# Kernel optimization log

Hardware: AMD Instinct MI355X
Metric: run time of the kernel (lower is better)

The kernel has to match this reference:

```python
import jax, jax.numpy as jnp
import numpy as np

B, IN, OUT, HS, NBDA = 128, 256, 256, 512, 1

def setup_inputs() -> dict:
    key = jax.random.key(0)
    ks = jax.random.split(key, 16)
    d = {}
    d["inputs"] = jax.random.normal(ks[0], (B, IN), dtype=jnp.float32)
    d["hidden"] = jax.random.normal(ks[1], (B, HS), dtype=jnp.float32)
    d["hebb"] = jax.random.normal(ks[2], (B, HS, HS), dtype=jnp.float32) * 0.1
    # learned params (torch.nn.Linear: y = x @ W.T + b)
    d["i2h_w"] = jax.random.normal(ks[3], (HS, IN), dtype=jnp.float32) * (1.0 / np.sqrt(IN))
    d["i2h_b"] = jnp.zeros((HS,), dtype=jnp.float32)
    d["w"] = 0.01 * jax.random.uniform(ks[4], (HS, HS), dtype=jnp.float32)
    d["alpha"] = 0.01 * jax.random.uniform(ks[5], (HS, HS), dtype=jnp.float32)
    d["h2o_w"] = jax.random.normal(ks[6], (OUT, HS), dtype=jnp.float32) * (1.0 / np.sqrt(HS))
    d["h2o_b"] = jnp.zeros((OUT,), dtype=jnp.float32)
    d["h2v_w"] = jax.random.normal(ks[7], (1, HS), dtype=jnp.float32) * (1.0 / np.sqrt(HS))
    d["h2v_b"] = jnp.zeros((1,), dtype=jnp.float32)
    d["h2da_w"] = jax.random.normal(ks[8], (NBDA, HS), dtype=jnp.float32) * (1.0 / np.sqrt(HS))
    d["h2da_b"] = jnp.zeros((NBDA,), dtype=jnp.float32)
    return d

def reference(inputs, hidden, hebb, i2h_w, i2h_b, w, alpha, h2o_w, h2o_b,
              h2v_w, h2v_b, h2da_w, h2da_b):
    # hactiv = tanh(i2h(x) + (w + alpha*hebb) @ hidden), per-sample weight matrix
    pre = inputs @ i2h_w.T + i2h_b                              # [B, HS]
    w_eff = w + alpha * hebb                                    # [B, HS, HS]
    rec = jnp.einsum('bij,bj->bi', w_eff, hidden)               # [B, HS]
    hactiv = jnp.tanh(pre + rec)                                # [B, HS]
    activout = hactiv @ h2o_w.T + h2o_b                         # [B, OUT]
    valueout = hactiv @ h2v_w.T + h2v_b                         # [B, 1]
    da = jnp.tanh(hactiv @ h2da_w.T + h2da_b)                   # [B, NBDA]
    # outer-product Hebbian update, DA-modulated, clamped to [-1, 1]
    deltahebb = hactiv[:, :, None] * hidden[:, None, :]         # [B, HS, HS]
    hebb_new = jnp.clip(hebb + da[:, :1, None] * deltahebb, -1.0, 1.0)
    return activout, valueout, hactiv, hebb_new
```

## Files before the change

### kernel.cpp

```cpp
#include <hip/hip_runtime.h>
#include <cstddef>
#include <cstdint>

#define B_    128
#define IN_   256
#define OUT_  256
#define HS_   512

#define NTHR_  512
#define NBLK_  1024

__device__ __forceinline__ float clip1(float x) {
    return fminf(fmaxf(x, -1.f), 1.f);
}

typedef float f32x4 __attribute__((ext_vector_type(4)));
__device__ __forceinline__ void nt_store4(float4* p, float4 v) {
    __builtin_nontemporal_store(*(f32x4*)&v, (f32x4*)p);
}

__global__ __launch_bounds__(NTHR_, 4) void k_pass1(
    const float* __restrict__ inputs,
    const float* __restrict__ hidden,
    const float* __restrict__ hebb,
    const float* __restrict__ i2h_w,
    const float* __restrict__ i2h_b,
    const float* __restrict__ w,
    const float* __restrict__ alpha,
    const float* __restrict__ h2v_w,
    const float* __restrict__ h2da_w,
    float* __restrict__ hactiv,
    float* __restrict__ ws_pd,
    float* __restrict__ ws_pv)
{
    const int blk  = blockIdx.x;
    const int b    = blk >> 3;
    const int s    = blk & 7;
    const int tid  = threadIdx.x;
    const int wave = tid >> 6;
    const int lane = tid & 63;
    const int r0   = s * 64 + wave * 8;

    __shared__ float s_pd[8], s_pv[8];

    const float4* hid4 = (const float4*)(hidden + (size_t)b * HS_);
    const float4 h0  = hid4[lane];
    const float4 h1  = hid4[lane + 64];
    const float4 in4 = ((const float4*)(inputs + (size_t)b * IN_))[lane];

    const float4* hb4 = (const float4*)hebb + ((size_t)b * HS_) * (HS_ / 4);
    const float4* w4  = (const float4*)w;
    const float4* a4  = (const float4*)alpha;
    const float4* iw4 = (const float4*)i2h_w;

    float pd = 0.f, pv = 0.f;
    for (int t = 0; t < 8; t += 2) {
        const int i = r0 + t;
        const float4* hpA = hb4 + (size_t)i * (HS_ / 4);
        const float4* hpB = hpA + (HS_ / 4);
        const float4* wpA = w4  + (size_t)i * (HS_ / 4);
        const float4* apA = a4  + (size_t)i * (HS_ / 4);
        const float4* ipA = iw4 + (size_t)i * (IN_ / 4);

        const float4 xA0 = hpA[lane],            xA1 = hpA[lane + 64];
        const float4 xB0 = hpB[lane],            xB1 = hpB[lane + 64];
        const float4 wA0 = wpA[lane],            wA1 = wpA[lane + 64];
        const float4 wB0 = wpA[128 + lane],      wB1 = wpA[128 + lane + 64];
        const float4 aA0 = apA[lane],            aA1 = apA[lane + 64];
        const float4 aB0 = apA[128 + lane],      aB1 = apA[128 + lane + 64];
        const float4 iA  = ipA[lane];
        const float4 iB  = ipA[64 + lane];

        float a, c;
        a  = (wA0.x + aA0.x * xA0.x) * h0.x;
        a += (wA0.y + aA0.y * xA0.y) * h0.y;
        a += (wA0.z + aA0.z * xA0.z) * h0.z;
        a += (wA0.w + aA0.w * xA0.w) * h0.w;
        a += (wA1.x + aA1.x * xA1.x) * h1.x;
        a += (wA1.y + aA1.y * xA1.y) * h1.y;
        a += (wA1.z + aA1.z * xA1.z) * h1.z;
        a += (wA1.w + aA1.w * xA1.w) * h1.w;
        a += iA.x * in4.x + iA.y * in4.y + iA.z * in4.z + iA.w * in4.w;

        c  = (wB0.x + aB0.x * xB0.x) * h0.x;
        c += (wB0.y + aB0.y * xB0.y) * h0.y;
        c += (wB0.z + aB0.z * xB0.z) * h0.z;
        c += (wB0.w + aB0.w * xB0.w) * h0.w;
        c += (wB1.x + aB1.x * xB1.x) * h1.x;
        c += (wB1.y + aB1.y * xB1.y) * h1.y;
        c += (wB1.z + aB1.z * xB1.z) * h1.z;
        c += (wB1.w + aB1.w * xB1.w) * h1.w;
        c += iB.x * in4.x + iB.y * in4.y + iB.z * in4.z + iB.w * in4.w;

        #pragma unroll
        for (int off = 1; off < 64; off <<= 1) {
            a += __shfl_xor(a, off, 64);
            c += __shfl_xor(c, off, 64);
        }

        const float hA = tanhf(a + i2h_b[i]);
        const float hB = tanhf(c + i2h_b[i + 1]);
        if (lane == 0) {
            float2* hp = (float2*)(hactiv + (size_t)b * HS_ + i);
            *hp = make_float2(hA, hB);
            pd += hA * h2da_w[i] + hB * h2da_w[i + 1];
            pv += hA * h2v_w[i]  + hB * h2v_w[i + 1];
        }
    }

    if (lane == 0) { s_pd[wave] = pd; s_pv[wave] = pv; }
    __syncthreads();
    if (tid == 0) {
        float sd = 0.f, sv = 0.f;
        #pragma unroll
        for (int k = 0; k < 8; ++k) { sd += s_pd[k]; sv += s_pv[k]; }
        ws_pd[b * 8 + s] = sd;
        ws_pv[b * 8 + s] = sv;
    }
}

__global__ __launch_bounds__(NTHR_, 4) void k_pass2(
    const float* __restrict__ hidden,
    const float* __restrict__ hebb,
    const float* __restrict__ h2o_w,
    const float* __restrict__ h2o_b,
    const float* __restrict__ h2v_b,
    const float* __restrict__ h2da_b,
    const float* __restrict__ hactiv,
    float* __restrict__ activout,
    float* __restrict__ valueout,
    float* __restrict__ hebb_new,
    const float* __restrict__ ws_pd,
    const float* __restrict__ ws_pv)
{
    const int blk  = blockIdx.x;
    const int b    = blk >> 3;
    const int s    = blk & 7;
    const int tid  = threadIdx.x;
    const int wave = tid >> 6;
    const int lane = tid & 63;
    const int r0   = s * 64 + wave * 8;

    __shared__ float s_h[HS_];
    __shared__ float s_part[512];
    __shared__ float s_bc[1];

    if (tid < 128)
        ((float4*)s_h)[tid] = ((const float4*)(hactiv + (size_t)b * HS_))[tid];
    if (tid == 0) {
        float sd = 0.f, sv = 0.f;
        #pragma unroll
        for (int k = 0; k < 8; ++k) {
            sd += ws_pd[b * 8 + k];
            sv += ws_pv[b * 8 + k];
        }
        s_bc[0] = tanhf(sd + h2da_b[0]);
        if (s == 0)
            valueout[b] = sv + h2v_b[0];
    }
    __syncthreads();
    const float da_b = s_bc[0];

    const float4* hid4 = (const float4*)(hidden + (size_t)b * HS_);
    const float4 h0 = hid4[lane];
    const float4 h1 = hid4[lane + 64];

    const float4* hb4 = (const float4*)hebb + ((size_t)b * HS_) * (HS_ / 4);

    for (int t = 0; t < 8; t += 2) {
        const int i = r0 + t;
        const float4* xp = hb4 + (size_t)i * (HS_ / 4);
        const float4 x0 = xp[lane],       x1 = xp[lane + 64];
        const float4 y0 = xp[128 + lane], y1 = xp[128 + lane + 64];
        const float scA = da_b * s_h[i];
        const float scB = da_b * s_h[i + 1];

        float4 o0, o1, p0, p1;
        o0.x = clip1(fmaf(scA, h0.x, x0.x));
        o0.y = clip1(fmaf(scA, h0.y, x0.y));
        o0.z = clip1(fmaf(scA, h0.z, x0.z));
        o0.w = clip1(fmaf(scA, h0.w, x0.w));
        o1.x = clip1(fmaf(scA, h1.x, x1.x));
        o1.y = clip1(fmaf(scA, h1.y, x1.y));
        o1.z = clip1(fmaf(scA, h1.z, x1.z));
        o1.w = clip1(fmaf(scA, h1.w, x1.w));
        p0.x = clip1(fmaf(scB, h0.x, y0.x));
        p0.y = clip1(fmaf(scB, h0.y, y0.y));
        p0.z = clip1(fmaf(scB, h0.z, y0.z));
        p0.w = clip1(fmaf(scB, h0.w, y0.w));
        p1.x = clip1(fmaf(scB, h1.x, y1.x));
        p1.y = clip1(fmaf(scB, h1.y, y1.y));
        p1.z = clip1(fmaf(scB, h1.z, y1.z));
        p1.w = clip1(fmaf(scB, h1.w, y1.w));

        float4* dp = (float4*)hebb_new + ((size_t)b * HS_ + i) * (HS_ / 4);
        nt_store4(dp + lane,            o0);
        nt_store4(dp + lane + 64,       o1);
        nt_store4(dp + 128 + lane,      p0);
        nt_store4(dp + 128 + lane + 64, p1);
    }

    {
        const int ol = tid & 31;
        const int sg = tid >> 5;
        const int o  = s * 32 + ol;
        const float4* wp  = (const float4*)(h2o_w + (size_t)o * HS_);
        const float4* hp4 = (const float4*)s_h;
        float acc = 0.f;
        #pragma unroll
        for (int c2 = 0; c2 < 8; ++c2) {
            const float4 wv = wp[sg * 8 + c2];
            const float4 hv = hp4[sg * 8 + c2];
            acc += wv.x * hv.x + wv.y * hv.y + wv.z * hv.z + wv.w * hv.w;
        }
        s_part[sg * 32 + ol] = acc;
    }
    __syncthreads();
    if (tid < 32) {
        const int o = s * 32 + tid;
        float acc = h2o_b[o];
        #pragma unroll
        for (int k = 0; k < 16; ++k)
            acc += s_part[k * 32 + tid];
        activout[(size_t)b * OUT_ + o] = acc;
    }
}

__global__ __launch_bounds__(256) void k1_hactiv(
    const float* __restrict__ inputs, const float* __restrict__ hidden,
    const float* __restrict__ hebb, const float* __restrict__ i2h_w,
    const float* __restrict__ i2h_b, const float* __restrict__ w,
    const float* __restrict__ alpha, float* __restrict__ hactiv)
{
    const int b     = blockIdx.x & (B_ - 1);
    const int chunk = blockIdx.x >> 7;
    const int tid   = threadIdx.x;
    const int wave  = tid >> 6;
    const int lane  = tid & 63;

    const float4* hid4 = (const float4*)(hidden + (size_t)b * HS_);
    const float4  h0   = hid4[lane];
    const float4  h1   = hid4[lane + 64];
    const float4  in4  = ((const float4*)(inputs + (size_t)b * IN_))[lane];

    const int i0 = chunk * 64 + wave * 16;

    for (int r = 0; r < 16; ++r) {
        const int i = i0 + r;
        const float4* hb = (const float4*)(hebb + ((size_t)b * HS_ + i) * HS_);
        const float4* wr = (const float4*)(w     + (size_t)i * HS_);
        const float4* ar = (const float4*)(alpha + (size_t)i * HS_);

        const float4 hb0 = hb[lane];
        const float4 hb1 = hb[lane + 64];
        const float4 wv0 = wr[lane];
        const float4 wv1 = wr[lane + 64];
        const float4 av0 = ar[lane];
        const float4 av1 = ar[lane + 64];
        const float4 iw  = ((const float4*)(i2h_w + (size_t)i * IN_))[lane];

        float acc;
        acc  = (wv0.x + av0.x * hb0.x) * h0.x;
        acc += (wv0.y + av0.y * hb0.y) * h0.y;
        acc += (wv0.z + av0.z * hb0.z) * h0.z;
        acc += (wv0.w + av0.w * hb0.w) * h0.w;
        acc += (wv1.x + av1.x * hb1.x) * h1.x;
        acc += (wv1.y + av1.y * hb1.y) * h1.y;
        acc += (wv1.z + av1.z * hb1.z) * h1.z;
        acc += (wv1.w + av1.w * hb1.w) * h1.w;
        acc += iw.x * in4.x + iw.y * in4.y + iw.z * in4.z + iw.w * in4.w;

        #pragma unroll
        for (int off = 32; off > 0; off >>= 1)
            acc += __shfl_down(acc, off, 64);

        if (lane == 0)
            hactiv[(size_t)b * HS_ + i] = tanhf(acc + i2h_b[i]);
    }
}

__global__ __launch_bounds__(256) void k2_heads(
    const float* __restrict__ hactiv, const float* __restrict__ h2o_w,
    const float* __restrict__ h2o_b, const float* __restrict__ h2v_w,
    const float* __restrict__ h2v_b, const float* __restrict__ h2da_w,
    const float* __restrict__ h2da_b, float* __restrict__ activout,
    float* __restrict__ valueout, float* __restrict__ da)
{
    const int b   = blockIdx.x;
    const int tid = threadIdx.x;

    __shared__ float s_h[HS_];
    __shared__ float red_v[256];
    __shared__ float red_d[256];

    for (int t = tid; t < HS_; t += 256)
        s_h[t] = hactiv[(size_t)b * HS_ + t];
    __syncthreads();

    const float4* wr  = (const float4*)(h2o_w + (size_t)tid * HS_);
    const float4* sh4 = (const float4*)s_h;
    float acc = 0.f;
    #pragma unroll 4
    for (int q = 0; q < HS_ / 4; ++q) {
        const float4 wv = wr[q];
        const float4 hv = sh4[q];
        acc += wv.x * hv.x + wv.y * hv.y + wv.z * hv.z + wv.w * hv.w;
    }
    activout[(size_t)b * OUT_ + tid] = acc + h2o_b[tid];

    float pv = 0.f, pd = 0.f;
    for (int t = tid; t < HS_; t += 256) {
        const float hv = s_h[t];
        pv += hv * h2v_w[t];
        pd += hv * h2da_w[t];
    }
    red_v[tid] = pv;
    red_d[tid] = pd;
    __syncthreads();
    for (int s2 = 128; s2 > 0; s2 >>= 1) {
        if (tid < s2) {
            red_v[tid] += red_v[tid + s2];
            red_d[tid] += red_d[tid + s2];
        }
        __syncthreads();
    }
    if (tid == 0) {
        valueout[b] = red_v[0] + h2v_b[0];
        da[b]       = tanhf(red_d[0] + h2da_b[0]);
    }
}

__global__ __launch_bounds__(256) void k3_hebb(
    const float* __restrict__ hebb, const float* __restrict__ hidden,
    const float* __restrict__ hactiv, const float* __restrict__ da,
    float* __restrict__ hebb_new)
{
    const int tid = threadIdx.x;
    const size_t base = (size_t)blockIdx.x * 1024;

    #pragma unroll
    for (int k = 0; k < 4; ++k) {
        const size_t idx = base + (size_t)k * 256 + tid;
        const int j4  = (int)(idx & 127);
        const int row = (int)(idx >> 7);
        const int i   = row & (HS_ - 1);
        const int b   = row >> 9;

        const float scale = da[b] * hactiv[(size_t)b * HS_ + i];
        const float4 hv = ((const float4*)hebb)[idx];
        const float4 hd = ((const float4*)hidden)[(size_t)b * (HS_ / 4) + j4];

        float4 r;
        r.x = fminf(fmaxf(fmaf(scale, hd.x, hv.x), -1.f), 1.f);
        r.y = fminf(fmaxf(fmaf(scale, hd.y, hv.y), -1.f), 1.f);
        r.z = fminf(fmaxf(fmaf(scale, hd.z, hv.z), -1.f), 1.f);
        r.w = fminf(fmaxf(fmaf(scale, hd.w, hv.w), -1.f), 1.f);
        ((float4*)hebb_new)[idx] = r;
    }
}

extern "C" void kernel_launch(void* const* d_in, const int* in_sizes, int n_in,
                              void* d_out, int out_size, void* d_ws, size_t ws_size,
                              hipStream_t stream)
{
    const float* inputs = (const float*)d_in[0];
    const float* hidden = (const float*)d_in[1];
    const float* hebb   = (const float*)d_in[2];
    const float* i2h_w  = (const float*)d_in[3];
    const float* i2h_b  = (const float*)d_in[4];
    const float* w      = (const float*)d_in[5];
    const float* alpha  = (const float*)d_in[6];
    const float* h2o_w  = (const float*)d_in[7];
    const float* h2o_b  = (const float*)d_in[8];
    const float* h2v_w  = (const float*)d_in[9];
    const float* h2v_b  = (const float*)d_in[10];
    const float* h2da_w = (const float*)d_in[11];
    const float* h2da_b = (const float*)d_in[12];

    float* out = (float*)d_out;
    float* activout = out;
    float* valueout = out + 32768;
    float* hactiv   = out + 32768 + 128;
    float* hebb_new = out + 32768 + 128 + 65536;

    const size_t part_bytes = (size_t)(2 * B_ * 8) * sizeof(float);

    if (ws_size >= part_bytes) {
        float* ws_pd = (float*)d_ws;
        float* ws_pv = ws_pd + B_ * 8;

        k_pass1<<<dim3(NBLK_), dim3(NTHR_), 0, stream>>>(
            inputs, hidden, hebb, i2h_w, i2h_b, w, alpha,
            h2v_w, h2da_w, hactiv, ws_pd, ws_pv);

        k_pass2<<<dim3(NBLK_), dim3(NTHR_), 0, stream>>>(
            hidden, hebb, h2o_w, h2o_b, h2v_b, h2da_b,
            hactiv, activout, valueout, hebb_new, ws_pd, ws_pv);
    } else {
        float* da = (float*)d_ws;
        k1_hactiv<<<dim3(1024), dim3(256), 0, stream>>>(
            inputs, hidden, hebb, i2h_w, i2h_b, w, alpha, hactiv);
        k2_heads<<<dim3(B_), dim3(256), 0, stream>>>(
            hactiv, h2o_w, h2o_b, h2v_w, h2v_b, h2da_w, h2da_b,
            activout, valueout, da);
        k3_hebb<<<dim3(8192), dim3(256), 0, stream>>>(
            hebb, hidden, hactiv, da, hebb_new);
    }
}
```

Measured before the change: 285.5 us.

## Hoist batch-shared W@h and i2h GEMM into tiled pre-kernel

Adds a small tiled GEMM kernel that computes i2h(x) + w@hidden once for the whole batch into a workspace buffer. The per-sample pass then only streams alpha and hebb, no longer rereading w and i2h_w in every block. This cuts redundant per-block loads of shared weights, at the cost of an extra launch and a low-occupancy 64-block GEMM. Pass2 also reads hactiv scalars from registers before the hebb loop and delays the shared-memory fill and barrier until after it. The new path only runs when the workspace is large enough; otherwise it falls back to the old fused pass1.

```diff
diff --git a/kernel.cpp b/kernel.cpp
--- a/kernel.cpp
+++ b/kernel.cpp
@@ -19,19 +19,154 @@
     __builtin_nontemporal_store(*(f32x4*)&v, (f32x4*)p);
 }
 
-__global__ __launch_bounds__(NTHR_, 4) void k_pass1(
+__global__ __launch_bounds__(256) void k0_pre(
     const float* __restrict__ inputs,
     const float* __restrict__ hidden,
-    const float* __restrict__ hebb,
     const float* __restrict__ i2h_w,
     const float* __restrict__ i2h_b,
     const float* __restrict__ w,
+    float* __restrict__ pre)
+{
+    const int it  = blockIdx.x & 15;
+    const int bt  = blockIdx.x >> 4;
+    const int tid = threadIdx.x;
+    const int il  = tid & 31;
+    const int bg  = tid >> 5;
+
+    __shared__ float Xl[32][68];
+    __shared__ float Wl[32][68];
+
+    float acc0 = 0.f, acc1 = 0.f, acc2 = 0.f, acc3 = 0.f;
+
+    for (int ck = 0; ck < 12; ++ck) {
+        __syncthreads();
+        #pragma unroll
+        for (int r = 0; r < 2; ++r) {
+            const int f   = tid + 256 * r;
+            const int row = f >> 4;
+            const int kf  = f & 15;
+            float4 xv, wv;
+            if (ck < 8) {
+                xv = *(const float4*)(hidden + (size_t)(bt*32 + row)*HS_ + ck*64 + kf*4);
+                wv = *(const float4*)(w      + (size_t)(it*32 + row)*HS_ + ck*64 + kf*4);
+            } else {
+                xv = *(const float4*)(inputs + (size_t)(bt*32 + row)*IN_ + (ck-8)*64 + kf*4);
+                wv = *(const float4*)(i2h_w  + (size_t)(it*32 + row)*IN_ + (ck-8)*64 + kf*4);
+            }
+            *(float4*)&Xl[row][kf*4] = xv;
+            *(float4*)&Wl[row][kf*4] = wv;
+        }
+        __syncthreads();
+        #pragma unroll
+        for (int kk = 0; kk < 64; ++kk) {
+            const float wv = Wl[il][kk];
+            acc0 = fmaf(wv, Xl[bg     ][kk], acc0);
+            acc1 = fmaf(wv, Xl[bg +  8][kk], acc1);
+            acc2 = fmaf(wv, Xl[bg + 16][kk], acc2);
+            acc3 = fmaf(wv, Xl[bg + 24][kk], acc3);
+        }
+    }
+
+    const int i = it * 32 + il;
+    const float bias = i2h_b[i];
+    pre[(size_t)(bt*32 + bg     ) * HS_ + i] = acc0 + bias;
+    pre[(size_t)(bt*32 + bg +  8) * HS_ + i] = acc1 + bias;
+    pre[(size_t)(bt*32 + bg + 16) * HS_ + i] = acc2 + bias;
+    pre[(size_t)(bt*32 + bg + 24) * HS_ + i] = acc3 + bias;
+}
+
+__global__ __launch_bounds__(NTHR_, 4) void k_pass1_slim(
+    const float* __restrict__ hidden,
+    const float* __restrict__ hebb,
     const float* __restrict__ alpha,
+    const float* __restrict__ pre,
     const float* __restrict__ h2v_w,
     const float* __restrict__ h2da_w,
     float* __restrict__ hactiv,
     float* __restrict__ ws_pd,
     float* __restrict__ ws_pv)
+{
+    const int blk  = blockIdx.x;
+    const int b    = blk >> 3;
+    const int s    = blk & 7;
+    const int tid  = threadIdx.x;
+    const int wave = tid >> 6;
+    const int lane = tid & 63;
+    const int r0   = s * 64 + wave * 8;
+
+    __shared__ float s_pd[8], s_pv[8];
+
+    const float4* hid4 = (const float4*)(hidden + (size_t)b * HS_);
+    const float4 h0 = hid4[lane];
+    const float4 h1 = hid4[lane + 64];
+
+    const float4* hb4 = (const float4*)hebb + ((size_t)b * HS_) * (HS_ / 4);
+    const float4* a4  = (const float4*)alpha;
+
+    float pd = 0.f, pv = 0.f;
+    for (int t = 0; t < 8; t += 2) {
+        const int i = r0 + t;
+        const float4* hpA = hb4 + (size_t)i * (HS_ / 4);
+        const float4* apA = a4  + (size_t)i * (HS_ / 4);
+
+        const float4 xA0 = hpA[lane],        xA1 = hpA[lane + 64];
+        const float4 xB0 = hpA[128 + lane],  xB1 = hpA[128 + lane + 64];
+        const float4 aA0 = apA[lane],        aA1 = apA[lane + 64];
+        const float4 aB0 = apA[128 + lane],  aB1 = apA[128 + lane + 64];
+
+        float a, c;
+        a  = (aA0.x * xA0.x) * h0.x;
+        a += (aA0.y * xA0.y) * h0.y;
+        a += (aA0.z * xA0.z) * h0.z;
+        a += (aA0.w * xA0.w) * h0.w;
+        a += (aA1.x * xA1.x) * h1.x;
+        a += (aA1.y * xA1.y) * h1.y;
+        a += (aA1.z * xA1.z) * h1.z;
+        a += (aA1.w * xA1.w) * h1.w;
+
+        c  = (aB0.x * xB0.x) * h0.x;
+        c += (aB0.y * xB0.y) * h0.y;
+        c += (aB0.z * xB0.z) * h0.z;
+        c += (aB0.w * xB0.w) * h0.w;
+        c += (aB1.x * xB1.x) * h1.x;
+        c += (aB1.y * xB1.y) * h1.y;
+        c += (aB1.z * xB1.z) * h1.z;
+        c += (aB1.w * xB1.w) * h1.w;
+
+        #pragma unroll
+        for (int off = 1; off < 64; off <<= 1) {
+            a += __shfl_xor(a, off, 64);
+            c += __shfl_xor(c, off, 64);
+        }
+
+        const float hA = tanhf(a + pre[(size_t)b * HS_ + i]);
+        const float hB = tanhf(c + pre[(size_t)b * HS_ + i + 1]);
+        if (lane == 0) {
+            float2* hp = (float2*)(hactiv + (size_t)b * HS_ + i);
+            *hp = make_float2(hA, hB);
+            pd += hA * h2da_w[i] + hB * h2da_w[i + 1];
+            pv += hA * h2v_w[i]  + hB * h2v_w[i + 1];
+        }
+    }
+
+    if (lane == 0) { s_pd[wave] = pd; s_pv[wave] = pv; }
+    __syncthreads();
+    if (tid == 0) {
+        float sd = 0.f, sv = 0.f;
+        #pragma unroll
+        for (int k = 0; k < 8; ++k) { sd += s_pd[k]; sv += s_pv[k]; }
+        ws_pd[b * 8 + s] = sd;
+        ws_pv[b * 8 + s] = sv;
+    }
+}
+
+__global__ __launch_bounds__(NTHR_, 4) void k_pass1_full(
+    const float* __restrict__ inputs, const float* __restrict__ hidden,
+    const float* __restrict__ hebb, const float* __restrict__ i2h_w,
+    const float* __restrict__ i2h_b, const float* __restrict__ w,
+    const float* __restrict__ alpha, const float* __restrict__ h2v_w,
+    const float* __restrict__ h2da_w, float* __restrict__ hactiv,
+    float* __restrict__ ws_pd, float* __restrict__ ws_pv)
 {
     const int blk  = blockIdx.x;
     const int b    = blk >> 3;
@@ -137,29 +272,27 @@
     const int b    = blk >> 3;
     const int s    = blk & 7;
     const int tid  = threadIdx.x;
+    const int lane = tid & 63;
     const int wave = tid >> 6;
-    const int lane = tid & 63;
     const int r0   = s * 64 + wave * 8;
 
     __shared__ float s_h[HS_];
     __shared__ float s_part[512];
-    __shared__ float s_bc[1];
-
-    if (tid < 128)
-        ((float4*)s_h)[tid] = ((const float4*)(hactiv + (size_t)b * HS_))[tid];
-    if (tid == 0) {
-        float sd = 0.f, sv = 0.f;
-        #pragma unroll
-        for (int k = 0; k < 8; ++k) {
-            sd += ws_pd[b * 8 + k];
-            sv += ws_pv[b * 8 + k];
-        }
-        s_bc[0] = tanhf(sd + h2da_b[0]);
-        if (s == 0)
-            valueout[b] = sv + h2v_b[0];
-    }
-    __syncthreads();
-    const float da_b = s_bc[0];
+
+    float sd = 0.f, sv = 0.f;
+    #pragma unroll
+    for (int k = 0; k < 8; ++k) {
+        sd += ws_pd[b * 8 + k];
+        sv += ws_pv[b * 8 + k];
+    }
+    const float da_b = tanhf(sd + h2da_b[0]);
+    if (s == 0 && tid == 0)
+        valueout[b] = sv + h2v_b[0];
+
+    float hr[8];
+    #pragma unroll
+    for (int q = 0; q < 8; ++q)
+        hr[q] = hactiv[(size_t)b * HS_ + r0 + q];
 
     const float4* hid4 = (const float4*)(hidden + (size_t)b * HS_);
     const float4 h0 = hid4[lane];
@@ -172,8 +305,8 @@
         const float4* xp = hb4 + (size_t)i * (HS_ / 4);
         const float4 x0 = xp[lane],       x1 = xp[lane + 64];
         const float4 y0 = xp[128 + lane], y1 = xp[128 + lane + 64];
-        const float scA = da_b * s_h[i];
-        const float scB = da_b * s_h[i + 1];
+        const float scA = da_b * hr[t];
+        const float scB = da_b * hr[t + 1];
 
         float4 o0, o1, p0, p1;
         o0.x = clip1(fmaf(scA, h0.x, x0.x));
@@ -200,6 +333,10 @@
         nt_store4(dp + 128 + lane + 64, p1);
     }
 
+    if (tid < 128)
+        ((float4*)s_h)[tid] = ((const float4*)(hactiv + (size_t)b * HS_))[tid];
+    __syncthreads();
+
     {
         const int ol = tid & 31;
         const int sg = tid >> 5;
@@ -384,12 +521,27 @@
     float* hebb_new = out + 32768 + 128 + 65536;
 
     const size_t part_bytes = (size_t)(2 * B_ * 8) * sizeof(float);
-
-    if (ws_size >= part_bytes) {
+    const size_t big_bytes  = part_bytes + (size_t)(B_ * HS_) * sizeof(float);
+
+    if (ws_size >= big_bytes) {
         float* ws_pd = (float*)d_ws;
         float* ws_pv = ws_pd + B_ * 8;
-
-        k_pass1<<<dim3(NBLK_), dim3(NTHR_), 0, stream>>>(
+        float* pre   = ws_pv + B_ * 8;
+
+        k0_pre<<<dim3(64), dim3(256), 0, stream>>>(
+            inputs, hidden, i2h_w, i2h_b, w, pre);
+
+        k_pass1_slim<<<dim3(NBLK_), dim3(NTHR_), 0, stream>>>(
+            hidden, hebb, alpha, pre, h2v_w, h2da_w, hactiv, ws_pd, ws_pv);
+
+        k_pass2<<<dim3(NBLK_), dim3(NTHR_), 0, stream>>>(
+            hidden, hebb, h2o_w, h2o_b, h2v_b, h2da_b,
+            hactiv, activout, valueout, hebb_new, ws_pd, ws_pv);
+    } else if (ws_size >= part_bytes) {
+        float* ws_pd = (float*)d_ws;
+        float* ws_pv = ws_pd + B_ * 8;
+
+        k_pass1_full<<<dim3(NBLK_), dim3(NTHR_), 0, stream>>>(
             inputs, hidden, hebb, i2h_w, i2h_b, w, alpha,
             h2v_w, h2da_w, hactiv, ws_pd, ws_pv);
 
```

After: 326.9 us. 14.5% more time.
